# Performance work log

Hardware: AMD Instinct MI355X
Metric: run time of the kernel (lower is better)

The kernel has to match this reference:

```python
import jax, jax.numpy as jnp
import numpy as np

COMMITMENT_COST = 0.25
ENTROPY_LOSS_WEIGHT = 0.1
EPSILON = 1e-05
NUM_EMBEDDINGS = 2048
EMBEDDING_DIM = 64


def setup_inputs() -> dict:
    key = jax.random.key(0)
    kx, ke = jax.random.split(key)
    x = jax.random.normal(kx, (16, 64, 64, EMBEDDING_DIM), dtype=jnp.float32)
    embedding = jax.random.normal(ke, (NUM_EMBEDDINGS, EMBEDDING_DIM), dtype=jnp.float32)
    return {"x": x, "embedding": embedding}


def reference(x, embedding):
    input_shape = x.shape
    flat_x = x.reshape(-1, EMBEDDING_DIM)              # [N, D]
    distances = (jnp.sum(flat_x ** 2, axis=1, keepdims=True)
                 + jnp.sum(embedding ** 2, axis=1)
                 - 2.0 * jnp.matmul(flat_x, embedding.T))
    encoding_indices = jnp.argmin(distances, axis=1)   # [N]
    quantized = embedding[encoding_indices].reshape(input_shape)

    commitment_loss = jnp.mean((jax.lax.stop_gradient(quantized) - x) ** 2)
    codebook_loss = jnp.mean((quantized - jax.lax.stop_gradient(x)) ** 2)
    # straight-through estimator
    quantized = x + jax.lax.stop_gradient(quantized - x)

    # histogram of code usage == mean of one-hot encodings (scatter-add, avoids [N,K] one-hot)
    n_tokens = flat_x.shape[0]
    counts = jnp.zeros((NUM_EMBEDDINGS,), dtype=flat_x.dtype).at[encoding_indices].add(1.0)
    avg_probs = counts / n_tokens
    perplexity = jnp.exp(-jnp.sum(avg_probs * jnp.log(avg_probs + EPSILON)))
    entropy_loss = jnp.sum(avg_probs * jnp.log(avg_probs + EPSILON))

    vq_loss = codebook_loss + COMMITMENT_COST * commitment_loss + ENTROPY_LOSS_WEIGHT * entropy_loss
    return (quantized, vq_loss, commitment_loss, codebook_loss, perplexity,
            entropy_loss, encoding_indices.reshape(input_shape[:-1]), avg_probs)
```

## Files before the change

kernel.cpp:

```cpp
#include <hip/hip_runtime.h>
#include <float.h>

typedef _Float16 half8 __attribute__((ext_vector_type(8)));
typedef float    f32x4 __attribute__((ext_vector_type(4)));

constexpr int N_TOK = 65536;
constexpr int D     = 64;
constexpr int K     = 2048;
constexpr int TILE_C = 64;
constexpr int NTILE  = K / TILE_C;
constexpr int TOK_PER_BLK = 64;
constexpr int NBLK = N_TOK / TOK_PER_BLK;
constexpr float EPS_RESCORE = 2e-3f;

constexpr size_t QN       = (size_t)N_TOK * D;
constexpr size_t SCAL_OFF = QN;
constexpr size_t IDX_OFF  = QN + 5;
constexpr size_t PROB_OFF = IDX_OFF + N_TOK;

constexpr size_t WS_HNORM = 0;
constexpr size_t WS_COUNT = 8192;
constexpr size_t WS_BSUM  = 16384;
constexpr size_t WS_SW    = 24576;

__device__ inline unsigned long long pack_key(float d, int k) {
    unsigned u = __float_as_uint(d);
    u = (u & 0x80000000u) ? ~u : (u | 0x80000000u);
    return ((unsigned long long)u << 32) | (unsigned)k;
}

__device__ inline float unpack_dist(unsigned long long key) {
    unsigned u = (unsigned)(key >> 32);
    u = (u & 0x80000000u) ? (u & 0x7FFFFFFFu) : ~u;
    return __uint_as_float(u);
}

__device__ inline unsigned long long shfl_xor_u64_w16(unsigned long long v, int m) {
    int lo = __shfl_xor((int)(unsigned)v, m, 16);
    int hi = __shfl_xor((int)(unsigned)(v >> 32), m, 16);
    return ((unsigned long long)(unsigned)hi << 32) | (unsigned)lo;
}

__global__ __launch_bounds__(256) void vq_init(const float* __restrict__ emb,
                                               float* __restrict__ hnorm,
                                               unsigned* __restrict__ counts,
                                               double* __restrict__ blocksums,
                                               half8* __restrict__ sw) {
    const int g  = blockIdx.x * 256 + threadIdx.x;
    const int r  = g >> 3;
    const int c0 = g & 7;
    const float4* p4 = (const float4*)(emb + (size_t)r * D + 8 * c0);
    float4 q0 = p4[0], q1 = p4[1];
    float v[8] = {q0.x, q0.y, q0.z, q0.w, q1.x, q1.y, q1.z, q1.w};
    half8 h, l;
    float s = 0.f;
#pragma unroll
    for (int i = 0; i < 8; ++i) {
        s += v[i] * v[i];
        _Float16 hh = (_Float16)v[i];
        h[i] = hh;
        l[i] = (_Float16)(v[i] - (float)hh);
    }
    const int t    = r >> 6;
    const int w    = (r >> 4) & 3;
    const int m16  = r & 15;
    const int lane = (c0 & 3) * 16 + m16;
    const int slot = c0 >> 2;
    half8* dst = sw + ((size_t)(t * 256 + w * 64 + lane)) * 4;
    dst[slot]     = h;
    dst[2 + slot] = l;

#pragma unroll
    for (int off = 1; off < 8; off <<= 1) s += __shfl_xor(s, off, 8);
    if (c0 == 0) hnorm[r] = 0.5f * s;
    if (g < K) counts[g] = 0u;
    if (g < NBLK) blocksums[g] = 0.0;
}

#define LOADB(TOFF, P0, P1, P2, P3, HN)                                            \
  {                                                                                \
    const half8* _q = pb + (TOFF) * 1024;                                          \
    P0 = _q[0]; P1 = _q[1]; P2 = _q[2]; P3 = _q[3];                                \
    HN = ph[(TOFF) * 64];                                                          \
  }

#define VQ_STEP(P0, P1, P2, P3, HN, TT)                                            \
  {                                                                                \
    f32x4 acc[4];                                                                  \
    __builtin_amdgcn_s_setprio(1);                                                 \
    _Pragma("unroll")                                                              \
    for (int a = 0; a < 4; ++a) {                                                  \
      acc[a] = (f32x4){(HN), (HN), (HN), (HN)};                                    \
      acc[a] = __builtin_amdgcn_mfma_f32_16x16x32_f16(axh[a][0], P0, acc[a], 0, 0, 0); \
      acc[a] = __builtin_amdgcn_mfma_f32_16x16x32_f16(axh[a][1], P1, acc[a], 0, 0, 0); \
      acc[a] = __builtin_amdgcn_mfma_f32_16x16x32_f16(axl[a][0], P0, acc[a], 0, 0, 0); \
      acc[a] = __builtin_amdgcn_mfma_f32_16x16x32_f16(axl[a][1], P1, acc[a], 0, 0, 0); \
      acc[a] = __builtin_amdgcn_mfma_f32_16x16x32_f16(axh[a][0], P2, acc[a], 0, 0, 0); \
      acc[a] = __builtin_amdgcn_mfma_f32_16x16x32_f16(axh[a][1], P3, acc[a], 0, 0, 0); \
    }                                                                              \
    __builtin_amdgcn_s_setprio(0);                                                 \
    _Pragma("unroll")                                                              \
    for (int a = 0; a < 4; ++a)                                                    \
      _Pragma("unroll")                                                            \
      for (int r = 0; r < 4; ++r) {                                                \
        unsigned _kb = (__float_as_uint(acc[a][r]) & 0xFFFFFFE0u) | (unsigned)(TT);\
        best_d[a][r] = fminf(best_d[a][r], __uint_as_float(_kb));                  \
      }                                                                            \
  }

__global__ __launch_bounds__(256) void vq_fused(const float* __restrict__ x,
                                                const float* __restrict__ emb,
                                                const float* __restrict__ hnorm,
                                                const half8* __restrict__ sw,
                                                unsigned* __restrict__ counts,
                                                double* __restrict__ blocksums,
                                                float* __restrict__ out) {
    __shared__ unsigned long long kls[64][5];
    __shared__ int bks[64];
    __shared__ double wsum[4];

    const int tid  = threadIdx.x;
    const int lane = tid & 63;
    const int wav  = tid >> 6;
    const int t0   = blockIdx.x * TOK_PER_BLK;
    const int m16  = lane & 15;
    const int g    = lane >> 4;
    const int ko   = g * 8;
    const int cit  = wav * 16 + m16;

    half8 axh[4][2], axl[4][2];
#pragma unroll
    for (int a = 0; a < 4; ++a) {
        const float* xr = x + (size_t)(t0 + 16 * a + m16) * D;
#pragma unroll
        for (int c = 0; c < 2; ++c) {
            const float4* p4 = (const float4*)(xr + 32 * c + ko);
            float4 q0 = p4[0], q1 = p4[1];
            float v[8] = {q0.x, q0.y, q0.z, q0.w, q1.x, q1.y, q1.z, q1.w};
            half8 h, l;
#pragma unroll
            for (int j = 0; j < 8; ++j) {
                float nv = -v[j];
                _Float16 hh = (_Float16)nv;
                h[j] = hh;
                l[j] = (_Float16)(nv - (float)hh);
            }
            axh[a][c] = h; axl[a][c] = l;
        }
    }

    float best_d[4][4];
#pragma unroll
    for (int a = 0; a < 4; ++a)
#pragma unroll
        for (int r = 0; r < 4; ++r) best_d[a][r] = FLT_MAX;

    const half8* pb = sw + (size_t)tid * 4;
    const float* ph = hnorm + cit;

    half8 sA0, sA1, sA2, sA3;  float hA;
    half8 sB0, sB1, sB2, sB3;  float hB;
    half8 sC0, sC1, sC2, sC3;  float hC;

    LOADB(0, sA0, sA1, sA2, sA3, hA);
    LOADB(1, sB0, sB1, sB2, sB3, hB);

    for (int t = 0; t < 28; t += 3) {
        LOADB(2, sC0, sC1, sC2, sC3, hC);
        VQ_STEP(sA0, sA1, sA2, sA3, hA, t);
        LOADB(3, sA0, sA1, sA2, sA3, hA);
        VQ_STEP(sB0, sB1, sB2, sB3, hB, t + 1);
        LOADB(4, sB0, sB1, sB2, sB3, hB);
        VQ_STEP(sC0, sC1, sC2, sC3, hC, t + 2);
        pb += 3 * 1024; ph += 3 * 64;
    }
    VQ_STEP(sA0, sA1, sA2, sA3, hA, 30);
    VQ_STEP(sB0, sB1, sB2, sB3, hB, 31);

#pragma unroll
    for (int a = 0; a < 4; ++a)
#pragma unroll
        for (int r = 0; r < 4; ++r) {
            const unsigned bits = __float_as_uint(best_d[a][r]);
            const int code = (int)(bits & 31u) * TILE_C + cit;
            unsigned long long key = pack_key(best_d[a][r], code);
#pragma unroll
            for (int off = 8; off; off >>= 1) {
                unsigned long long o = shfl_xor_u64_w16(key, off);
                if (o < key) key = o;
            }
            if (m16 == 0) kls[16 * a + g * 4 + r][wav] = key;
        }
    __syncthreads();

    if (tid < 64) {
        float ds[4]; int kk[4];
        unsigned long long kmin = ~0ULL;
#pragma unroll
        for (int w = 0; w < 4; ++w) {
            unsigned long long key = kls[tid][w];
            ds[w] = unpack_dist(key);
            kk[w] = (int)(unsigned)(key & 0xFFFFFFFFu);
            if (key < kmin) kmin = key;
        }
        int bk = (int)(unsigned)(kmin & 0xFFFFFFFFu);
        const float fmin = unpack_dist(kmin);
        int cnt = 0;
#pragma unroll
        for (int w = 0; w < 4; ++w) cnt += (ds[w] <= fmin + EPS_RESCORE) ? 1 : 0;

        if (cnt > 1) {
            unsigned long long bkey = ~0ULL;
            const float* xr = x + (size_t)(t0 + tid) * D;
            for (int w = 0; w < 4; ++w) {
                if (ds[w] <= fmin + EPS_RESCORE) {
                    const int k = kk[w];
                    const float* cr = emb + (size_t)k * D;
                    float s0 = 0.f, s1 = 0.f, s2 = 0.f, s3 = 0.f;
#pragma unroll
                    for (int i = 0; i < 16; ++i) {
                        s0 = fmaf(cr[4 * i + 0], xr[4 * i + 0], s0);
                        s1 = fmaf(cr[4 * i + 1], xr[4 * i + 1], s1);
                        s2 = fmaf(cr[4 * i + 2], xr[4 * i + 2], s2);
                        s3 = fmaf(cr[4 * i + 3], xr[4 * i + 3], s3);
                    }
                    float hd = hnorm[k] - ((s0 + s1) + (s2 + s3));
                    unsigned long long key = pack_key(hd, k);
                    if (key < bkey) bkey = key;
                }
            }
            bk = (int)(unsigned)(bkey & 0xFFFFFFFFu);
        }
        bks[tid] = bk;
        out[IDX_OFF + t0 + tid] = (float)bk;
        atomicAdd(&counts[bk], 1u);
    }
    __syncthreads();

    const int tok = tid >> 2;
    const int i4  = tid & 3;
    const int bk  = bks[tok];
    const float4* xr4 = (const float4*)(x + (size_t)(t0 + tok) * D);
    const float4* cr4 = (const float4*)(emb + (size_t)bk * D);
    float4* qr4 = (float4*)(out + (size_t)(t0 + tok) * D);
    float local = 0.f;
#pragma unroll
    for (int ii = 0; ii < 4; ++ii) {
        const int idx = i4 + 4 * ii;
        float4 xv = xr4[idx];
        float4 cv = cr4[idx];
        float dx = cv.x - xv.x, dy = cv.y - xv.y;
        float dz = cv.z - xv.z, dw = cv.w - xv.w;
        local += dx * dx + dy * dy + dz * dz + dw * dw;
        float4 q;
        q.x = xv.x + dx; q.y = xv.y + dy;
        q.z = xv.z + dz; q.w = xv.w + dw;
        qr4[idx] = q;
    }
    double ld = (double)local;
#pragma unroll
    for (int off = 32; off > 0; off >>= 1) ld += __shfl_down(ld, off, 64);
    if (lane == 0) wsum[wav] = ld;
    __syncthreads();
    if (tid == 0)
        blocksums[blockIdx.x] = (wsum[0] + wsum[1]) + (wsum[2] + wsum[3]);
}

__global__ __launch_bounds__(256) void vq_finalize(const unsigned* __restrict__ counts,
                                                   const double* __restrict__ blocksums,
                                                   float* __restrict__ out) {
    const int tid = threadIdx.x;
    double e = 0.0;
#pragma unroll
    for (int i = 0; i < 8; ++i) {
        int k = tid + i * 256;
        float p = (float)counts[k] / 65536.0f;
        out[PROB_OFF + k] = p;
        double pd = (double)p;
        e += pd * log(pd + 1e-5);
    }
    double s = 0.0;
#pragma unroll
    for (int i = 0; i < NBLK / 256; ++i) s += blocksums[tid + i * 256];
#pragma unroll
    for (int off = 32; off > 0; off >>= 1) {
        e += __shfl_down(e, off, 64);
        s += __shfl_down(s, off, 64);
    }
    __shared__ double we[4], ws2[4];
    int lane = tid & 63, wid = tid >> 6;
    if (lane == 0) { we[wid] = e; ws2[wid] = s; }
    __syncthreads();
    if (tid == 0) {
        double entropy = (we[0] + we[1]) + (we[2] + we[3]);
        double sumsq   = (ws2[0] + ws2[1]) + (ws2[2] + ws2[3]);
        double mse     = sumsq / (double)((size_t)N_TOK * D);
        out[SCAL_OFF + 0] = (float)(1.25 * mse + 0.1 * entropy);
        out[SCAL_OFF + 1] = (float)mse;
        out[SCAL_OFF + 2] = (float)mse;
        out[SCAL_OFF + 3] = (float)exp(-entropy);
        out[SCAL_OFF + 4] = (float)entropy;
    }
}

extern "C" void kernel_launch(void* const* d_in, const int* in_sizes, int n_in,
                              void* d_out, int out_size, void* d_ws, size_t ws_size,
                              hipStream_t stream) {
    const float* x   = (const float*)d_in[0];
    const float* emb = (const float*)d_in[1];
    float* out = (float*)d_out;

    char* ws = (char*)d_ws;
    float*    hnorm     = (float*)(ws + WS_HNORM);
    unsigned* counts    = (unsigned*)(ws + WS_COUNT);
    double*   blocksums = (double*)(ws + WS_BSUM);
    half8*    sw        = (half8*)(ws + WS_SW);

    vq_init<<<K * 8 / 256, 256, 0, stream>>>(emb, hnorm, counts, blocksums, sw);
    vq_fused<<<NBLK, 256, 0, stream>>>(x, emb, hnorm, sw, counts, blocksums, out);
    vq_finalize<<<1, 256, 0, stream>>>(counts, blocksums, out);
}
```

Measured before the change: 133.9 us.

## Split MFMA accumulation chains and stagger codebook tile order per block

Each distance tile is now accumulated into two independent MFMA accumulators that are summed afterwards, which shortens the dependent MFMA chain and removes the setprio hints. Each block starts its codebook tile sweep at a hashed offset, so concurrent blocks read different tiles and contend less on the same cache lines. The prefetch depth drops from triple to double buffering. The extra adds and lower prefetch depth may cost latency hiding, and the tie-breaking order between equal distances is unchanged because the tile index stays encoded in the key bits.

```diff
diff --git a/kernel.cpp b/kernel.cpp
--- a/kernel.cpp
+++ b/kernel.cpp
@@ -77,35 +77,32 @@
     if (g < NBLK) blocksums[g] = 0.0;
 }
 
-#define LOADB(TOFF, P0, P1, P2, P3, HN)                                            \
+#define LOADB(TT, P0, P1, P2, P3, HN)                                              \
   {                                                                                \
-    const half8* _q = pb + (TOFF) * 1024;                                          \
+    const half8* _q = pb0 + ((size_t)(TT) << 10);                                  \
     P0 = _q[0]; P1 = _q[1]; P2 = _q[2]; P3 = _q[3];                                \
-    HN = ph[(TOFF) * 64];                                                          \
+    HN = ph0[(TT) << 6];                                                           \
   }
 
 #define VQ_STEP(P0, P1, P2, P3, HN, TT)                                            \
   {                                                                                \
-    f32x4 acc[4];                                                                  \
-    __builtin_amdgcn_s_setprio(1);                                                 \
     _Pragma("unroll")                                                              \
     for (int a = 0; a < 4; ++a) {                                                  \
-      acc[a] = (f32x4){(HN), (HN), (HN), (HN)};                                    \
-      acc[a] = __builtin_amdgcn_mfma_f32_16x16x32_f16(axh[a][0], P0, acc[a], 0, 0, 0); \
-      acc[a] = __builtin_amdgcn_mfma_f32_16x16x32_f16(axh[a][1], P1, acc[a], 0, 0, 0); \
-      acc[a] = __builtin_amdgcn_mfma_f32_16x16x32_f16(axl[a][0], P0, acc[a], 0, 0, 0); \
-      acc[a] = __builtin_amdgcn_mfma_f32_16x16x32_f16(axl[a][1], P1, acc[a], 0, 0, 0); \
-      acc[a] = __builtin_amdgcn_mfma_f32_16x16x32_f16(axh[a][0], P2, acc[a], 0, 0, 0); \
-      acc[a] = __builtin_amdgcn_mfma_f32_16x16x32_f16(axh[a][1], P3, acc[a], 0, 0, 0); \
-    }                                                                              \
-    __builtin_amdgcn_s_setprio(0);                                                 \
-    _Pragma("unroll")                                                              \
-    for (int a = 0; a < 4; ++a)                                                    \
+      f32x4 ac1 = {(HN), (HN), (HN), (HN)};                                        \
+      f32x4 ac2 = {0.f, 0.f, 0.f, 0.f};                                            \
+      ac1 = __builtin_amdgcn_mfma_f32_16x16x32_f16(axh[a][0], P0, ac1, 0, 0, 0);   \
+      ac2 = __builtin_amdgcn_mfma_f32_16x16x32_f16(axh[a][1], P1, ac2, 0, 0, 0);   \
+      ac1 = __builtin_amdgcn_mfma_f32_16x16x32_f16(axl[a][0], P0, ac1, 0, 0, 0);   \
+      ac2 = __builtin_amdgcn_mfma_f32_16x16x32_f16(axl[a][1], P1, ac2, 0, 0, 0);   \
+      ac1 = __builtin_amdgcn_mfma_f32_16x16x32_f16(axh[a][0], P2, ac1, 0, 0, 0);   \
+      ac2 = __builtin_amdgcn_mfma_f32_16x16x32_f16(axh[a][1], P3, ac2, 0, 0, 0);   \
       _Pragma("unroll")                                                            \
       for (int r = 0; r < 4; ++r) {                                                \
-        unsigned _kb = (__float_as_uint(acc[a][r]) & 0xFFFFFFE0u) | (unsigned)(TT);\
+        float _d = ac1[r] + ac2[r];                                                \
+        unsigned _kb = (__float_as_uint(_d) & 0xFFFFFFE0u) | (unsigned)(TT);       \
         best_d[a][r] = fminf(best_d[a][r], __uint_as_float(_kb));                  \
       }                                                                            \
+    }                                                                              \
   }
 
 __global__ __launch_bounds__(256) void vq_fused(const float* __restrict__ x,
@@ -155,27 +152,27 @@
 #pragma unroll
         for (int r = 0; r < 4; ++r) best_d[a][r] = FLT_MAX;
 
-    const half8* pb = sw + (size_t)tid * 4;
-    const float* ph = hnorm + cit;
+    const half8* pb0 = sw + (size_t)tid * 4;
+    const float* ph0 = hnorm + cit;
+
+    const int b = blockIdx.x;
+    const int tstart = (b ^ (b >> 5) ^ (b >> 8)) & 31;
 
     half8 sA0, sA1, sA2, sA3;  float hA;
     half8 sB0, sB1, sB2, sB3;  float hB;
-    half8 sC0, sC1, sC2, sC3;  float hC;
-
-    LOADB(0, sA0, sA1, sA2, sA3, hA);
-    LOADB(1, sB0, sB1, sB2, sB3, hB);
-
-    for (int t = 0; t < 28; t += 3) {
-        LOADB(2, sC0, sC1, sC2, sC3, hC);
-        VQ_STEP(sA0, sA1, sA2, sA3, hA, t);
-        LOADB(3, sA0, sA1, sA2, sA3, hA);
-        VQ_STEP(sB0, sB1, sB2, sB3, hB, t + 1);
-        LOADB(4, sB0, sB1, sB2, sB3, hB);
-        VQ_STEP(sC0, sC1, sC2, sC3, hC, t + 2);
-        pb += 3 * 1024; ph += 3 * 64;
-    }
-    VQ_STEP(sA0, sA1, sA2, sA3, hA, 30);
-    VQ_STEP(sB0, sB1, sB2, sB3, hB, 31);
+
+    int ttA = tstart;
+    LOADB(ttA, sA0, sA1, sA2, sA3, hA);
+
+    for (int i = 0; i < NTILE; i += 2) {
+        const int ttB = (tstart + i + 1) & 31;
+        LOADB(ttB, sB0, sB1, sB2, sB3, hB);
+        VQ_STEP(sA0, sA1, sA2, sA3, hA, ttA);
+        const int ttN = (tstart + i + 2) & 31;
+        if (i + 2 < NTILE) { LOADB(ttN, sA0, sA1, sA2, sA3, hA); }
+        VQ_STEP(sB0, sB1, sB2, sB3, hB, ttB);
+        ttA = ttN;
+    }
 
 #pragma unroll
     for (int a = 0; a < 4; ++a)
```

Measured after the change: 134.2 us. No clear change (+0.2%).
